# Kernel tuning notes

Hardware: AMD Instinct MI355X
Metric: run time of the kernel (lower is better)

Reference implementation:

```python
import jax, jax.numpy as jnp
import numpy as np

B, C, H, W = 4, 2048, 48, 48
HC = 256

def setup_inputs() -> dict:
    key = jax.random.key(0)
    k1, k2, k3, k4 = jax.random.split(key, 4)
    scale = 1.0 / np.sqrt(C)
    return {
        "left_features": jax.random.normal(k1, (B, C, H, W), dtype=jnp.float32),
        "right_features": jax.random.normal(k2, (B, C, H, W), dtype=jnp.float32),
        "Wq": jax.random.normal(k3, (HC, C), dtype=jnp.float32) * scale,
        "bq": jnp.zeros((HC,), dtype=jnp.float32),
        "Wk": jax.random.normal(k4, (HC, C), dtype=jnp.float32) * scale,
        "bk": jnp.zeros((HC,), dtype=jnp.float32),
    }

def _coattn(query_feat, ref_feat, Wq, bq, Wk, bk):
    b, c, h, w = query_feat.shape
    hw = h * w
    # 1x1 convs == per-pixel channel projections
    Q = jnp.einsum('bchw,oc->bohw', query_feat, Wq) + bq[None, :, None, None]
    K = jnp.einsum('bchw,oc->bohw', ref_feat, Wk) + bk[None, :, None, None]
    Qf = Q.reshape(b, -1, hw)          # [b, hc, hw_q]
    Kf = K.reshape(b, -1, hw)          # [b, hc, hw_k]
    V = ref_feat.reshape(b, c, hw)     # [b, c, hw_k]
    # attention scores over all spatial pairs, softmax over reference positions
    attn = jax.nn.softmax(jnp.einsum('bci,bcj->bij', Qf, Kf), axis=-1)  # [b, hw_q, hw_k]
    out = jnp.einsum('bij,bcj->bci', attn, V)  # [b, c, hw_q]
    return out.reshape(b, c, h, w)

def reference(left_features, right_features, Wq, bq, Wk, bk):
    weighted_r = _coattn(left_features, right_features, Wq, bq, Wk, bk)
    weighted_l = _coattn(right_features, left_features, Wq, bq, Wk, bk)
    # rearrange '[orig, weighted] two b c h w -> b (two c) h w' == channel concat
    left_attended = jnp.concatenate([left_features, weighted_l], axis=1)
    right_attended = jnp.concatenate([right_features, weighted_r], axis=1)
    return (left_attended, right_attended)
```

## Files before the change

### kernel.cpp

```cpp
#include <hip/hip_runtime.h>
#include <stdint.h>


#define NB 4
#define NC 2048
#define NHW 2304
#define NHC 256
#define NT 36

typedef _Float16 f16;
typedef __attribute__((ext_vector_type(4))) _Float16 f16x4;
typedef __attribute__((ext_vector_type(8))) _Float16 f16x8;
typedef __attribute__((ext_vector_type(4))) float f32x4;

static __device__ __forceinline__ void glds16(const void* g, void* lds) {
  __builtin_amdgcn_global_load_lds(
      (const __attribute__((address_space(1))) uint32_t*)g,
      (__attribute__((address_space(3))) uint32_t*)lds, 16, 0, 0);
}

__global__ __launch_bounds__(256) void k_prep(
    const float* __restrict__ xl, const float* __restrict__ xr,
    float* __restrict__ out, f16* __restrict__ Xh, f16* __restrict__ Xt) {
  const int z = blockIdx.z, side = z >> 2, b = z & 3;
  const float* X = (side ? xr : xl) + (size_t)b * NC * NHW;
  const int hw0 = blockIdx.x * 64, c0 = blockIdx.y * 64;
  const int t = threadIdx.x;
  const int colb = (t & 15) * 4;
  const int r0 = t >> 4;
  __shared__ f16 Lt[64 * 64];
  float* outb = out + (size_t)side * ((size_t)NB * 2 * NC * NHW) + (size_t)b * (2 * NC * NHW);
  f16* Xhb = Xh + (size_t)side * ((size_t)NB * NC * NHW) + (size_t)b * NC * NHW;
  f16* Xtb = Xt + (size_t)side * ((size_t)NB * NHW * NC) + (size_t)b * NHW * NC;
#pragma unroll
  for (int p = 0; p < 4; ++p) {
    int r = r0 + p * 16;
    size_t go = (size_t)(c0 + r) * NHW + hw0 + colb;
    float4 v = *(const float4*)&X[go];
    *(float4*)&outb[go] = v;
    f16x4 h; h[0] = (f16)v.x; h[1] = (f16)v.y; h[2] = (f16)v.z; h[3] = (f16)v.w;
    *(f16x4*)&Xhb[go] = h;
#pragma unroll
    for (int j = 0; j < 4; ++j) {
      int row = colb + j;
      int byte = row * 128 + ((r * 2) ^ ((((row >> 2) & 7)) << 4));
      *(f16*)((char*)Lt + byte) = h[j];
    }
  }
  __syncthreads();
#pragma unroll
  for (int p = 0; p < 2; ++p) {
    int idx = p * 256 + t;
    int row = idx >> 3, ch = idx & 7;
    int byte = row * 128 + (((ch ^ ((row >> 2) & 7))) << 4);
    f16x8 vv = *(const f16x8*)((char*)Lt + byte);
    *(f16x8*)&Xtb[(size_t)(hw0 + row) * NC + c0 + ch * 8] = vv;
  }
}

__global__ __launch_bounds__(256) void k_w16(
    const float* __restrict__ wq, const float* __restrict__ wk, f16* __restrict__ Ws) {
  const int N4 = NHC * NC / 4;
  int idx = blockIdx.x * 256 + threadIdx.x;
  const float* src = (idx < N4) ? wq : wk;
  int e4 = (idx < N4) ? idx : idx - N4;
  float4 v = ((const float4*)src)[e4];
  f16x4 h; h[0] = (f16)v.x; h[1] = (f16)v.y; h[2] = (f16)v.z; h[3] = (f16)v.w;
  ((f16x4*)Ws)[idx] = h;
}

__global__ __launch_bounds__(256) void k_proj(
    const f16* __restrict__ Ws, const f16* __restrict__ Xt,
    const float* __restrict__ bq, const float* __restrict__ bk,
    f16* __restrict__ Yt) {
  __shared__ f16 LA[2][128 * 32], LB[2][128 * 32];
  const int n0 = blockIdx.x * 128;
  const int m0 = blockIdx.y * 128;
  const int tid = threadIdx.x, wv = tid >> 6, ln = tid & 63;
  const int lr = ln & 15, lh = ln >> 4;
  const int wm = wv >> 1, wn = wv & 1;
  f32x4 acc[4][4];
#pragma unroll
  for (int mi = 0; mi < 4; ++mi)
#pragma unroll
    for (int ni = 0; ni < 4; ++ni)
#pragma unroll
      for (int q = 0; q < 4; ++q) acc[mi][ni][q] = 0.f;

  auto stage = [&](int bi, int ks) {
    int k0 = ks * 32;
#pragma unroll
    for (int rep = 0; rep < 2; ++rep) {
      int u = rep * 256 + wv * 64 + ln;
      int r = u >> 2, k8 = (u & 3) * 8;
      int ub8 = (rep * 256 + wv * 64) * 8;
      glds16(Ws + (size_t)(m0 + r) * NC + k0 + k8, &LA[bi][ub8]);
      glds16(Xt + (size_t)(n0 + r) * NC + k0 + k8, &LB[bi][ub8]);
    }
  };
  auto compute = [&](int bi) {
    f16x8 af[4], bf[4];
#pragma unroll
    for (int mi = 0; mi < 4; ++mi)
      af[mi] = *(const f16x8*)&LA[bi][(wm * 64 + mi * 16 + lr) * 32 + lh * 8];
#pragma unroll
    for (int ni = 0; ni < 4; ++ni)
      bf[ni] = *(const f16x8*)&LB[bi][(wn * 64 + ni * 16 + lr) * 32 + lh * 8];
#pragma unroll
    for (int mi = 0; mi < 4; ++mi)
#pragma unroll
      for (int ni = 0; ni < 4; ++ni)
        acc[mi][ni] = __builtin_amdgcn_mfma_f32_16x16x32_f16(af[mi], bf[ni], acc[mi][ni], 0, 0, 0);
  };

  stage(0, 0);
  __syncthreads();
  int cur = 0;
  for (int ks = 0; ks < 63; ++ks) {
    stage(cur ^ 1, ks + 1);
    compute(cur);
    __syncthreads();
    cur ^= 1;
  }
  compute(cur);

#pragma unroll
  for (int mi = 0; mi < 4; ++mi)
#pragma unroll
    for (int ni = 0; ni < 4; ++ni) {
      int ob = m0 + wm * 64 + mi * 16 + lh * 4;
      int i = n0 + wn * 64 + ni * 16 + lr;
      f16x4 hv;
#pragma unroll
      for (int q = 0; q < 4; ++q) {
        int o = ob + q;
        float bias = (o < NHC) ? bq[o] : bk[o - NHC];
        hv[q] = (f16)(acc[mi][ni][q] + bias);
      }
      *(f16x4*)&Yt[(size_t)i * 512 + ob] = hv;
    }
}

__global__ __launch_bounds__(256) void k_scores(
    const f16* __restrict__ Q, const f16* __restrict__ K, float* __restrict__ S) {
  __shared__ f16 LA[2][128 * 32], LB[2][128 * 32];
  const int b = blockIdx.z;
  const int i0 = blockIdx.x * 128, j0 = blockIdx.y * 128;
  const int tid = threadIdx.x, wv = tid >> 6, ln = tid & 63;
  const int lr = ln & 15, lh = ln >> 4;
  const int wm = wv >> 1, wn = wv & 1;
  const f16* Qb = Q + (size_t)b * NHW * 512;
  const f16* Kb = K + (size_t)b * NHW * 512;
  f32x4 acc[4][4];
#pragma unroll
  for (int mi = 0; mi < 4; ++mi)
#pragma unroll
    for (int ni = 0; ni < 4; ++ni)
#pragma unroll
      for (int q = 0; q < 4; ++q) acc[mi][ni][q] = 0.f;

  auto stage = [&](int bi, int ks) {
    int k0 = ks * 32;
#pragma unroll
    for (int rep = 0; rep < 2; ++rep) {
      int u = rep * 256 + wv * 64 + ln;
      int r = u >> 2, k8 = (u & 3) * 8;
      int ub8 = (rep * 256 + wv * 64) * 8;
      glds16(Qb + (size_t)(i0 + r) * 512 + k0 + k8, &LA[bi][ub8]);
      glds16(Kb + (size_t)(j0 + r) * 512 + k0 + k8, &LB[bi][ub8]);
    }
  };
  auto compute = [&](int bi) {
    f16x8 af[4], bf[4];
#pragma unroll
    for (int mi = 0; mi < 4; ++mi)
      af[mi] = *(const f16x8*)&LA[bi][(wm * 64 + mi * 16 + lr) * 32 + lh * 8];
#pragma unroll
    for (int ni = 0; ni < 4; ++ni)
      bf[ni] = *(const f16x8*)&LB[bi][(wn * 64 + ni * 16 + lr) * 32 + lh * 8];
#pragma unroll
    for (int mi = 0; mi < 4; ++mi)
#pragma unroll
      for (int ni = 0; ni < 4; ++ni)
        acc[mi][ni] = __builtin_amdgcn_mfma_f32_16x16x32_f16(af[mi], bf[ni], acc[mi][ni], 0, 0, 0);
  };

  stage(0, 0);
  __syncthreads();
  int cur = 0;
  for (int ks = 0; ks < 7; ++ks) {
    stage(cur ^ 1, ks + 1);
    compute(cur);
    __syncthreads();
    cur ^= 1;
  }
  compute(cur);

  float* Sb = S + (size_t)b * NHW * NHW;
#pragma unroll
  for (int mi = 0; mi < 4; ++mi)
#pragma unroll
    for (int ni = 0; ni < 4; ++ni) {
      int i = i0 + wm * 64 + mi * 16 + lh * 4;
      int j = j0 + wn * 64 + ni * 16 + lr;
#pragma unroll
      for (int q = 0; q < 4; ++q)
        Sb[(size_t)(i + q) * NHW + j] = acc[mi][ni][q];
    }
}

__global__ __launch_bounds__(256) void k_softmax(float* __restrict__ S) {
  const int row = blockIdx.x;
  float* rp = S + (size_t)row * NHW;
  const int t = threadIdx.x;
  float v[9];
  float m = -3.4e38f;
#pragma unroll
  for (int k = 0; k < 9; ++k) { v[k] = rp[t + 256 * k]; m = fmaxf(m, v[k]); }
#pragma unroll
  for (int off = 32; off > 0; off >>= 1) m = fmaxf(m, __shfl_xor(m, off));
  __shared__ float red[4];
  __shared__ float red2[4];
  const int wv = t >> 6, ln = t & 63;
  if (ln == 0) red[wv] = m;
  __syncthreads();
  m = fmaxf(fmaxf(red[0], red[1]), fmaxf(red[2], red[3]));
  float s = 0.f;
#pragma unroll
  for (int k = 0; k < 9; ++k) { v[k] = expf(v[k] - m); s += v[k]; }
#pragma unroll
  for (int off = 32; off > 0; off >>= 1) s += __shfl_xor(s, off);
  if (ln == 0) red2[wv] = s;
  __syncthreads();
  float inv = 1.0f / (red2[0] + red2[1] + red2[2] + red2[3]);
  f16* op = (f16*)rp;
#pragma unroll
  for (int k = 0; k < 9; ++k) op[t + 256 * k] = (f16)(v[k] * inv);
}

__global__ __launch_bounds__(512, 2) void k_pv8(
    const f16* __restrict__ V0, const f16* __restrict__ V1,
    const float* __restrict__ S0, const float* __restrict__ S1,
    float* __restrict__ out, int ndirs, long long ob0, long long ob1) {
  extern __shared__ __align__(16) f16 SH[];
  f16* LA = SH;
  f16* LB = SH + 3 * 16384;

  const int nwg = ndirs * 576;
  const int bid = blockIdx.x;
  const int wg = (bid & 7) * (nwg >> 3) + (bid >> 3);
  const int n = wg % 18;
  const int r1 = wg / 18;
  const int m = r1 & 7;
  const int r2 = r1 >> 3;
  const int b = r2 & 3;
  const int dir = r2 >> 2;

  const f16* Vb = (dir ? V1 : V0) + (size_t)b * NC * NHW;
  const char* Sb = (const char*)(dir ? S1 : S0) + (size_t)b * NHW * NHW * 4;
  const long long obase = dir ? ob1 : ob0;
  const int c0 = m * 256, i0 = n * 128;
  const int tid = threadIdx.x, wv = tid >> 6, ln = tid & 63;
  const int lr = ln & 15, lg = ln >> 4;
  const int wm = wv >> 1, wn = wv & 1;

  const int fr = tid >> 3;
  const int scolb = ((tid & 7) * 16) ^ ((fr & 7) << 4);
  const f16* aSrc = Vb + (size_t)(c0 + fr) * NHW + (scolb >> 1);
  const char* bSrc = Sb + (size_t)(i0 + fr) * 9216 + scolb;
  const int ldsW = wv * 512;

  auto stA = [&](int s, int t2, int r) {
    glds16(aSrc + (size_t)r * 64 * NHW + t2 * 64, LA + s * 16384 + r * 4096 + ldsW);
  };
  auto stB = [&](int s, int t2, int r) {
    glds16(bSrc + (size_t)r * 64 * 9216 + t2 * 128, LB + s * 8192 + r * 4096 + ldsW);
  };
  auto rdA = [&](int s, int mi, int ks) -> f16x8 {
    int row = wm * 64 + mi * 16 + lr;
    int colb = (ks * 64 + lg * 16) ^ ((row & 7) << 4);
    return *(const f16x8*)((const char*)(LA + s * 16384) + row * 128 + colb);
  };
  auto rdB = [&](int s, int ni, int ks) -> f16x8 {
    int row = wn * 64 + ni * 16 + lr;
    int colb = (ks * 64 + lg * 16) ^ ((row & 7) << 4);
    return *(const f16x8*)((const char*)(LB + s * 8192) + row * 128 + colb);
  };

  f32x4 acc[4][4];
#pragma unroll
  for (int mi = 0; mi < 4; ++mi)
#pragma unroll
    for (int ni = 0; ni < 4; ++ni)
#pragma unroll
      for (int q = 0; q < 4; ++q) acc[mi][ni][q] = 0.f;

#pragma unroll
  for (int r = 0; r < 4; ++r) stA(0, 0, r);
  stB(0, 0, 0); stB(0, 0, 1);
#pragma unroll
  for (int r = 0; r < 4; ++r) stA(1, 1, r);
  stB(1, 1, 0); stB(1, 1, 1);
  asm volatile("s_waitcnt vmcnt(6)" ::: "memory");
  asm volatile("s_barrier" ::: "memory");

  int s = 0;
  for (int t = 0; t < NT; ++t) {
    int s2 = s + 2; if (s2 >= 3) s2 -= 3;
    const bool st = (t + 2 < NT);
    f16x8 bf[4][2], af[2][2];
#pragma unroll
    for (int ni = 0; ni < 4; ++ni) { bf[ni][0] = rdB(s, ni, 0); bf[ni][1] = rdB(s, ni, 1); }
#pragma unroll
    for (int mi = 0; mi < 2; ++mi) { af[mi][0] = rdA(s, mi, 0); af[mi][1] = rdA(s, mi, 1); }
    if (st) { stA(s2, t + 2, 0); stA(s2, t + 2, 1); stA(s2, t + 2, 2); }
    asm volatile("s_barrier" ::: "memory");
    __builtin_amdgcn_s_setprio(1);
#pragma unroll
    for (int ks = 0; ks < 2; ++ks)
#pragma unroll
      for (int mi = 0; mi < 2; ++mi)
#pragma unroll
        for (int ni = 0; ni < 4; ++ni)
          acc[mi][ni] = __builtin_amdgcn_mfma_f32_16x16x32_f16(af[mi][ks], bf[ni][ks], acc[mi][ni], 0, 0, 0);
    __builtin_amdgcn_s_setprio(0);
    asm volatile("s_barrier" ::: "memory");
    f16x8 a2[2][2];
#pragma unroll
    for (int mi = 0; mi < 2; ++mi) { a2[mi][0] = rdA(s, 2 + mi, 0); a2[mi][1] = rdA(s, 2 + mi, 1); }
    if (st) { stA(s2, t + 2, 3); stB(s2, t + 2, 0); stB(s2, t + 2, 1); }
    if (t < NT - 2) { asm volatile("s_waitcnt vmcnt(6)" ::: "memory"); }
    else            { asm volatile("s_waitcnt vmcnt(0)" ::: "memory"); }
    asm volatile("s_barrier" ::: "memory");
    __builtin_amdgcn_s_setprio(1);
#pragma unroll
    for (int ks = 0; ks < 2; ++ks)
#pragma unroll
      for (int mi = 0; mi < 2; ++mi)
#pragma unroll
        for (int ni = 0; ni < 4; ++ni)
          acc[2 + mi][ni] = __builtin_amdgcn_mfma_f32_16x16x32_f16(a2[mi][ks], bf[ni][ks], acc[2 + mi][ni], 0, 0, 0);
    __builtin_amdgcn_s_setprio(0);
    asm volatile("s_barrier" ::: "memory");
    s += 1; if (s == 3) s = 0;
  }

  float* ob = out + obase + (size_t)b * (2 * NC * NHW);
#pragma unroll
  for (int mi = 0; mi < 4; ++mi)
#pragma unroll
    for (int ni = 0; ni < 4; ++ni) {
      int c = c0 + wm * 64 + mi * 16 + lg * 4;
      int i = i0 + wn * 64 + ni * 16 + lr;
#pragma unroll
      for (int q = 0; q < 4; ++q)
        ob[(size_t)(NC + c + q) * NHW + i] = acc[mi][ni][q];
    }
}

extern "C" void kernel_launch(void* const* d_in, const int* in_sizes, int n_in,
                              void* d_out, int out_size, void* d_ws, size_t ws_size,
                              hipStream_t stream) {
  const float* xl = (const float*)d_in[0];
  const float* xr = (const float*)d_in[1];
  const float* wq = (const float*)d_in[2];
  const float* bq = (const float*)d_in[3];
  const float* wk = (const float*)d_in[4];
  const float* bk = (const float*)d_in[5];
  float* out = (float*)d_out;
  char* ws = (char*)d_ws;

  const size_t XH_BYTES = (size_t)2 * NB * NC * NHW * 2;
  const size_t WS_BYTES = (size_t)512 * NC * 2;
  const size_t YT_BYTES = (size_t)2 * NB * NHW * 512 * 2;
  const size_t S_BYTES  = (size_t)NB * NHW * NHW * 4;

  f16* Xh = (f16*)ws;
  f16* Ws_ = (f16*)(ws + XH_BYTES);
  f16* Yt = (f16*)(ws + XH_BYTES + WS_BYTES);
  char* rest = ws + XH_BYTES + WS_BYTES + YT_BYTES;

  const size_t xh_side = (size_t)NB * NC * NHW;
  const size_t xt_side = (size_t)NB * NHW * NC;
  const size_t yt_side = (size_t)NB * NHW * 512;
  const long long obA = (long long)NB * 2 * NC * NHW;
  const long long obB = 0;

  const bool merged = ws_size >= XH_BYTES + WS_BYTES + YT_BYTES + 2 * S_BYTES;

  if (merged) {
    float* S0 = (float*)rest;
    char* rest2 = rest + S_BYTES;
    f16* Xt = (f16*)rest2;
    float* S1 = (float*)rest2;

    k_prep<<<dim3(36, 32, 8), dim3(256), 0, stream>>>(xl, xr, out, Xh, Xt);
    k_w16<<<dim3(1024), dim3(256), 0, stream>>>(wq, wk, Ws_);
    k_proj<<<dim3(72, 4), dim3(256), 0, stream>>>(Ws_, Xt, bq, bk, Yt);
    k_proj<<<dim3(72, 4), dim3(256), 0, stream>>>(Ws_, Xt + xt_side, bq, bk, Yt + yt_side);

    k_scores<<<dim3(18, 18, NB), dim3(256), 0, stream>>>(Yt, Yt + yt_side + NHC, S0);
    k_scores<<<dim3(18, 18, NB), dim3(256), 0, stream>>>(Yt + yt_side, Yt + NHC, S1);
    k_softmax<<<dim3(NB * NHW), dim3(256), 0, stream>>>(S0);
    k_softmax<<<dim3(NB * NHW), dim3(256), 0, stream>>>(S1);
    k_pv8<<<dim3(1152), dim3(512), 147456, stream>>>(
        Xh + xh_side, Xh, S0, S1, out, 2, obA, obB);
  } else {
    f16* Xt = (f16*)rest;
    float* S = (float*)rest;

    k_prep<<<dim3(36, 32, 8), dim3(256), 0, stream>>>(xl, xr, out, Xh, Xt);
    k_w16<<<dim3(1024), dim3(256), 0, stream>>>(wq, wk, Ws_);
    k_proj<<<dim3(72, 4), dim3(256), 0, stream>>>(Ws_, Xt, bq, bk, Yt);
    k_proj<<<dim3(72, 4), dim3(256), 0, stream>>>(Ws_, Xt + xt_side, bq, bk, Yt + yt_side);

    k_scores<<<dim3(18, 18, NB), dim3(256), 0, stream>>>(Yt, Yt + yt_side + NHC, S);
    k_softmax<<<dim3(NB * NHW), dim3(256), 0, stream>>>(S);
    k_pv8<<<dim3(576), dim3(512), 147456, stream>>>(
        Xh + xh_side, Xh + xh_side, S, S, out, 1, obA, obA);

    k_scores<<<dim3(18, 18, NB), dim3(256), 0, stream>>>(Yt + yt_side, Yt + NHC, S);
    k_softmax<<<dim3(NB * NHW), dim3(256), 0, stream>>>(S);
    k_pv8<<<dim3(576), dim3(512), 147456, stream>>>(
        Xh, Xh, S, S, out, 1, obB, obB);
  }
}
```

Baseline: 504.8 us.

## Register double-buffer LDS fragments in PV GEMM and merge softmax launches

Restructures the k_pv8 main loop so the LDS fragments for the next K-step are read into a second register set while the current step's MFMAs run. This cuts the per-iteration phases from two barrier-separated halves to one, with all global-to-LDS stores issued up front. It also merges the two softmax launches into a single grid covering both score buffers, saving a launch. In exchange the GEMM holds twice as many A/B fragment registers, which raises register pressure and may lower occupancy.

Result: slower. 522.9 us (+3.6%).

```diff
diff --git a/kernel.cpp b/kernel.cpp
--- a/kernel.cpp
+++ b/kernel.cpp
@@ -209,9 +209,11 @@
     }
 }
 
-__global__ __launch_bounds__(256) void k_softmax(float* __restrict__ S) {
-  const int row = blockIdx.x;
-  float* rp = S + (size_t)row * NHW;
+__global__ __launch_bounds__(256) void k_softmax(
+    float* __restrict__ S0, float* __restrict__ S1) {
+  const int rid = blockIdx.x;
+  const int ROWS = NB * NHW;
+  float* rp = (rid < ROWS ? S0 : S1) + (size_t)(rid < ROWS ? rid : rid - ROWS) * NHW;
   const int t = threadIdx.x;
   float v[9];
   float m = -3.4e38f;
@@ -295,6 +297,8 @@
 #pragma unroll
       for (int q = 0; q < 4; ++q) acc[mi][ni][q] = 0.f;
 
+  f16x8 A0[4][2], B0[4][2], A1[4][2], B1[4][2];
+
 #pragma unroll
   for (int r = 0; r < 4; ++r) stA(0, 0, r);
   stB(0, 0, 0); stB(0, 0, 1);
@@ -303,46 +307,47 @@
   stB(1, 1, 0); stB(1, 1, 1);
   asm volatile("s_waitcnt vmcnt(6)" ::: "memory");
   asm volatile("s_barrier" ::: "memory");
-
-  int s = 0;
-  for (int t = 0; t < NT; ++t) {
+#pragma unroll
+  for (int mi = 0; mi < 4; ++mi) { A0[mi][0] = rdA(0, mi, 0); A0[mi][1] = rdA(0, mi, 1); }
+#pragma unroll
+  for (int ni = 0; ni < 4; ++ni) { B0[ni][0] = rdB(0, ni, 0); B0[ni][1] = rdB(0, ni, 1); }
+
+  auto step = [&](int t, int s, f16x8 (&Ac)[4][2], f16x8 (&Bc)[4][2],
+                  f16x8 (&Ap)[4][2], f16x8 (&Bp)[4][2]) {
     int s2 = s + 2; if (s2 >= 3) s2 -= 3;
-    const bool st = (t + 2 < NT);
-    f16x8 bf[4][2], af[2][2];
-#pragma unroll
-    for (int ni = 0; ni < 4; ++ni) { bf[ni][0] = rdB(s, ni, 0); bf[ni][1] = rdB(s, ni, 1); }
-#pragma unroll
-    for (int mi = 0; mi < 2; ++mi) { af[mi][0] = rdA(s, mi, 0); af[mi][1] = rdA(s, mi, 1); }
-    if (st) { stA(s2, t + 2, 0); stA(s2, t + 2, 1); stA(s2, t + 2, 2); }
+    int s1 = s + 1; if (s1 >= 3) s1 -= 3;
+    if (t + 2 < NT) {
+      stA(s2, t + 2, 0); stA(s2, t + 2, 1); stA(s2, t + 2, 2); stA(s2, t + 2, 3);
+      stB(s2, t + 2, 0); stB(s2, t + 2, 1);
+      asm volatile("s_waitcnt vmcnt(6)" ::: "memory");
+    } else {
+      asm volatile("s_waitcnt vmcnt(0)" ::: "memory");
+    }
     asm volatile("s_barrier" ::: "memory");
+    if (t + 1 < NT) {
+#pragma unroll
+      for (int mi = 0; mi < 4; ++mi) { Ap[mi][0] = rdA(s1, mi, 0); Ap[mi][1] = rdA(s1, mi, 1); }
+#pragma unroll
+      for (int ni = 0; ni < 4; ++ni) { Bp[ni][0] = rdB(s1, ni, 0); Bp[ni][1] = rdB(s1, ni, 1); }
+    }
     __builtin_amdgcn_s_setprio(1);
 #pragma unroll
     for (int ks = 0; ks < 2; ++ks)
 #pragma unroll
-      for (int mi = 0; mi < 2; ++mi)
+      for (int mi = 0; mi < 4; ++mi)
 #pragma unroll
         for (int ni = 0; ni < 4; ++ni)
-          acc[mi][ni] = __builtin_amdgcn_mfma_f32_16x16x32_f16(af[mi][ks], bf[ni][ks], acc[mi][ni], 0, 0, 0);
+          acc[mi][ni] = __builtin_amdgcn_mfma_f32_16x16x32_f16(Ac[mi][ks], Bc[ni][ks], acc[mi][ni], 0, 0, 0);
     __builtin_amdgcn_s_setprio(0);
     asm volatile("s_barrier" ::: "memory");
-    f16x8 a2[2][2];
-#pragma unroll
-    for (int mi = 0; mi < 2; ++mi) { a2[mi][0] = rdA(s, 2 + mi, 0); a2[mi][1] = rdA(s, 2 + mi, 1); }
-    if (st) { stA(s2, t + 2, 3); stB(s2, t + 2, 0); stB(s2, t + 2, 1); }
-    if (t < NT - 2) { asm volatile("s_waitcnt vmcnt(6)" ::: "memory"); }
-    else            { asm volatile("s_waitcnt vmcnt(0)" ::: "memory"); }
-    asm volatile("s_barrier" ::: "memory");
-    __builtin_amdgcn_s_setprio(1);
-#pragma unroll
-    for (int ks = 0; ks < 2; ++ks)
-#pragma unroll
-      for (int mi = 0; mi < 2; ++mi)
-#pragma unroll
-        for (int ni = 0; ni < 4; ++ni)
-          acc[2 + mi][ni] = __builtin_amdgcn_mfma_f32_16x16x32_f16(a2[mi][ks], bf[ni][ks], acc[2 + mi][ni], 0, 0, 0);
-    __builtin_amdgcn_s_setprio(0);
-    asm volatile("s_barrier" ::: "memory");
-    s += 1; if (s == 3) s = 0;
+  };
+
+  int s = 0;
+  for (int t = 0; t < NT; t += 2) {
+    step(t, s, A0, B0, A1, B1);
+    int sn = s + 1; if (sn >= 3) sn -= 3;
+    step(t + 1, sn, A1, B1, A0, B0);
+    s = s + 2; if (s >= 3) s -= 3;
   }
 
   float* ob = out + obase + (size_t)b * (2 * NC * NHW);
@@ -401,8 +406,7 @@
 
     k_scores<<<dim3(18, 18, NB), dim3(256), 0, stream>>>(Yt, Yt + yt_side + NHC, S0);
     k_scores<<<dim3(18, 18, NB), dim3(256), 0, stream>>>(Yt + yt_side, Yt + NHC, S1);
-    k_softmax<<<dim3(NB * NHW), dim3(256), 0, stream>>>(S0);
-    k_softmax<<<dim3(NB * NHW), dim3(256), 0, stream>>>(S1);
+    k_softmax<<<dim3(2 * NB * NHW), dim3(256), 0, stream>>>(S0, S1);
     k_pv8<<<dim3(1152), dim3(512), 147456, stream>>>(
         Xh + xh_side, Xh, S0, S1, out, 2, obA, obB);
   } else {
@@ -415,12 +419,12 @@
     k_proj<<<dim3(72, 4), dim3(256), 0, stream>>>(Ws_, Xt + xt_side, bq, bk, Yt + yt_side);
 
     k_scores<<<dim3(18, 18, NB), dim3(256), 0, stream>>>(Yt, Yt + yt_side + NHC, S);
-    k_softmax<<<dim3(NB * NHW), dim3(256), 0, stream>>>(S);
+    k_softmax<<<dim3(NB * NHW), dim3(256), 0, stream>>>(S, S);
     k_pv8<<<dim3(576), dim3(512), 147456, stream>>>(
         Xh + xh_side, Xh + xh_side, S, S, out, 1, obA, obA);
 
     k_scores<<<dim3(18, 18, NB), dim3(256), 0, stream>>>(Yt + yt_side, Yt + NHC, S);
-    k_softmax<<<dim3(NB * NHW), dim3(256), 0, stream>>>(S);
+    k_softmax<<<dim3(NB * NHW), dim3(256), 0, stream>>>(S, S);
     k_pv8<<<dim3(576), dim3(512), 147456, stream>>>(
         Xh, Xh, S, S, out, 1, obB, obB);
   }
```
